# Optimization experiments

Measured on AMD Instinct MI355X. Metric: run time of the kernel, lower is better.

The kernel has to match this reference:

```python
import jax, jax.numpy as jnp
import numpy as np

SCALE = 768.0  # scale = output_features


def setup_inputs() -> dict:
    key = jax.random.key(0)
    k1, k2, k3, k4 = jax.random.split(key, 4)
    B, S, D, F = 8, 2048, 768, 768
    x = jax.random.normal(k1, (B, S, D), dtype=jnp.float32)
    # torch nn.Linear weights: shape (out_features, in_features), y = x @ W.T
    Wq = jax.random.normal(k2, (F, D), dtype=jnp.float32) * (1.0 / np.sqrt(D))
    Wk = jax.random.normal(k3, (F, D), dtype=jnp.float32) * (1.0 / np.sqrt(D))
    Wv = jax.random.normal(k4, (F, D), dtype=jnp.float32) * (1.0 / np.sqrt(D))
    return {"x": x, "Wq": Wq, "Wk": Wk, "Wv": Wv}


def _cdist_l2(q, k):
    # pairwise Euclidean distances, [B, S, S]; matches torch.cdist(q, k, p=2)
    q2 = jnp.sum(q * q, axis=-1)  # [B, S]
    k2 = jnp.sum(k * k, axis=-1)  # [B, S]
    qk = jnp.einsum('bid,bjd->bij', q, k)  # [B, S, S]
    d2 = q2[:, :, None] + k2[:, None, :] - 2.0 * qk
    return jnp.sqrt(jnp.maximum(d2, 0.0))


def reference(x, Wq, Wk, Wv):
    q = jnp.einsum('bsd,fd->bsf', x, Wq)
    k = jnp.einsum('bsd,fd->bsf', x, Wk)
    v = jnp.einsum('bsd,fd->bsf', x, Wv)
    scores = _cdist_l2(q, k) / jnp.sqrt(jnp.asarray(SCALE, dtype=x.dtype))
    attn = jax.nn.softmax(scores, axis=-1)  # NOTE: source softmaxes raw distances (no negation)
    return jnp.einsum('bij,bjf->bif', attn, v)
```

## Files before the change

### kernel.cpp

```cpp
#include <hip/hip_runtime.h>
#include <stdint.h>
#include <math.h>


typedef __attribute__((ext_vector_type(8))) __bf16 bf16x8;
typedef __attribute__((ext_vector_type(4))) float f32x4;

__device__ __forceinline__ unsigned short f2b(float f) {
    unsigned u = __float_as_uint(f);
    unsigned r = 0x7fffu + ((u >> 16) & 1u);
    return (unsigned short)((u + r) >> 16);
}
__device__ __forceinline__ float b2f(unsigned short h) {
    return __uint_as_float(((unsigned)h) << 16);
}

__device__ __forceinline__ void wg_barrier() {
    asm volatile("" ::: "memory");
    __builtin_amdgcn_s_barrier();
    asm volatile("" ::: "memory");
}

__device__ __forceinline__ void glds16(const unsigned short* src, unsigned short* dst) {
    __builtin_amdgcn_global_load_lds(
        (const __attribute__((address_space(1))) unsigned int*)src,
        (__attribute__((address_space(3))) unsigned int*)dst, 16, 0, 0);
}

__device__ __forceinline__ unsigned lds_off(const void* p) {
    return (unsigned)(uintptr_t)(const __attribute__((address_space(3))) char*)p;
}

__global__ __launch_bounds__(256) void castk(const float* __restrict__ src,
                                             unsigned short* __restrict__ dst, int n4) {
    int i = blockIdx.x * 256 + threadIdx.x;
    if (i >= n4) return;
    float4 v = ((const float4*)src)[i];
    ushort4 o;
    o.x = f2b(v.x); o.y = f2b(v.y); o.z = f2b(v.z); o.w = f2b(v.w);
    ((ushort4*)dst)[i] = o;
}

template <int MODE>
__global__ __launch_bounds__(256) void rowreduce(const unsigned short* __restrict__ X,
                                                 int L, int rows, float* __restrict__ out) {
    int w = threadIdx.x >> 6, lane = threadIdx.x & 63;
    int row = blockIdx.x * 4 + w;
    if (row >= rows) return;
    const unsigned short* xr = X + (size_t)row * L;
    float s = 0.f;
    int passes = L >> 8;
    for (int p = 0; p < passes; ++p) {
        ushort4 u = *(const ushort4*)(xr + (p << 8) + lane * 4);
        float a = b2f(u.x), b = b2f(u.y), c = b2f(u.z), d = b2f(u.w);
        s += MODE ? (a * a + b * b + c * c + d * d) : (a + b + c + d);
    }
#pragma unroll
    for (int o = 32; o > 0; o >>= 1) s += __shfl_down(s, o);
    if (lane == 0) out[row] = s;
}

#define MF(A_, B_, C_) (C_) = __builtin_amdgcn_mfma_f32_16x16x32_bf16((A_), (B_), (C_), 0, 0, 0)
#define DSR(dst_, a_, imm_) \
    asm volatile("ds_read_b128 %0, %1 offset:" #imm_ : "=v"(dst_) : "v"(a_))
#define LGKM(n_) asm volatile("s_waitcnt lgkmcnt(" #n_ ")" ::: "memory")
#define VMC6 asm volatile("s_waitcnt vmcnt(6)" ::: "memory")
#define VMC0 asm volatile("s_waitcnt vmcnt(0)" ::: "memory")
#define SB0 __builtin_amdgcn_sched_barrier(0)
#define NOPS ((void)0)

#define CLUSTER(MI0_, NI0_, AARR_, BARR_)                                  \
    _Pragma("unroll") for (int mi_ = 0; mi_ < 4; ++mi_) {                  \
        _Pragma("unroll") for (int ni_ = 0; ni_ < 2; ++ni_) {              \
            MF(AARR_[mi_][0], BARR_[ni_][0], acc[(MI0_) + mi_][(NI0_) + ni_]); \
            MF(AARR_[mi_][1], BARR_[ni_][1], acc[(MI0_) + mi_][(NI0_) + ni_]); \
        }                                                                  \
    }

#define TILE(A0_, A0X_, B0_, B0X_, S1_, S2_, S3_, S4_, VMW_) do {          \
    DSR(aF[0][0], A0_, 0);    DSR(aF[0][1], A0X_, 0);                      \
    DSR(aF[1][0], A0_, 2048); DSR(aF[1][1], A0X_, 2048);                   \
    DSR(aF[2][0], A0_, 4096); DSR(aF[2][1], A0X_, 4096);                   \
    DSR(aF[3][0], A0_, 6144); DSR(aF[3][1], A0X_, 6144);                   \
    DSR(bL[0][0], B0_, 0);    DSR(bL[0][1], B0X_, 0);                      \
    DSR(bL[1][0], B0_, 2048); DSR(bL[1][1], B0X_, 2048);                   \
    S1_;                                                                   \
    LGKM(8);                                                               \
    wg_barrier();                                                          \
    LGKM(0); SB0;                                                          \
    __builtin_amdgcn_s_setprio(1);                                         \
    CLUSTER(0, 0, aF, bL)                                                  \
    SB0; __builtin_amdgcn_s_setprio(0);                                    \
    wg_barrier();                                                          \
    DSR(bH[0][0], B0_, 4096); DSR(bH[0][1], B0X_, 4096);                   \
    DSR(bH[1][0], B0_, 6144); DSR(bH[1][1], B0X_, 6144);                   \
    S2_;                                                                   \
    wg_barrier();                                                          \
    LGKM(0); SB0;                                                          \
    __builtin_amdgcn_s_setprio(1);                                         \
    CLUSTER(0, 2, aF, bH)                                                  \
    SB0; __builtin_amdgcn_s_setprio(0);                                    \
    wg_barrier();                                                          \
    DSR(aH[0][0], A0_, 8192);  DSR(aH[0][1], A0X_, 8192);                  \
    DSR(aH[1][0], A0_, 10240); DSR(aH[1][1], A0X_, 10240);                 \
    DSR(aH[2][0], A0_, 12288); DSR(aH[2][1], A0X_, 12288);                 \
    DSR(aH[3][0], A0_, 14336); DSR(aH[3][1], A0X_, 14336);                 \
    S3_;                                                                   \
    wg_barrier();                                                          \
    LGKM(0); SB0;                                                          \
    __builtin_amdgcn_s_setprio(1);                                         \
    CLUSTER(4, 2, aH, bH)                                                  \
    SB0; __builtin_amdgcn_s_setprio(0);                                    \
    wg_barrier();                                                          \
    S4_;                                                                   \
    VMW_;                                                                  \
    wg_barrier();                                                          \
    SB0;                                                                   \
    __builtin_amdgcn_s_setprio(1);                                         \
    CLUSTER(4, 0, aH, bL)                                                  \
    SB0; __builtin_amdgcn_s_setprio(0);                                    \
    wg_barrier();                                                          \
} while (0)

#define SA_(T_, BUF_, H_) do {                                             \
    const unsigned short* s_ = pA0 + (size_t)((H_) * 64) * lda + (size_t)(T_) * 64; \
    unsigned short* d_ = As + (BUF_) * 16384 + (H_) * 4096 + tid * 8;      \
    glds16(s_, d_);                                                        \
    glds16(s_ + (size_t)128 * lda, d_ + 8192);                             \
} while (0)
#define SBs_(T_, BUF_, H_) do {                                            \
    const unsigned short* s_ = pB0 + (size_t)((H_) * 32) * ldb + (size_t)(T_) * 64; \
    unsigned short* d_ = Bs + (BUF_) * 16384 + (H_) * 2048 + dB0 + tid * 8; \
    glds16(s_, d_);                                                        \
    glds16(s_ + (size_t)128 * ldb, d_ + 8192);                             \
} while (0)

template <int EPI>
__global__ __launch_bounds__(512, 2) void gemm256(
    const unsigned short* __restrict__ A, int lda, long long sA,
    const unsigned short* __restrict__ B, int ldb, long long sB,
    void* __restrict__ Cv, int ldc, long long sC,
    int Kd,
    const float* __restrict__ aux1, int sAux1,
    const float* __restrict__ aux2, int sAux2,
    float invs) {
    __shared__ __attribute__((aligned(128))) unsigned short As[2 * 256 * 64];
    __shared__ __attribute__((aligned(128))) unsigned short Bs[2 * 256 * 64];

    const int z = blockIdx.z;
    const unsigned short* __restrict__ Ab = A + (size_t)z * sA;
    const unsigned short* __restrict__ Bb = B + (size_t)z * sB;
    const int i0 = blockIdx.y * 256;
    const int j0 = blockIdx.x * 256;
    const int tid = threadIdx.x;
    const int w = tid >> 6, lane = tid & 63;
    const int wr = w >> 2, wc = w & 3;
    const int c16 = lane & 15, kq = lane >> 4;

    const int lr0 = tid >> 3;
    const int clog0 = (tid & 7) ^ (lr0 & 7);
    const unsigned short* pA0 = Ab + (size_t)(i0 + lr0) * lda + clog0 * 8;
    const unsigned short* pB0 = Bb + (size_t)(j0 + lr0 + (lr0 & 32)) * ldb + clog0 * 8;
    const int dB0 = (tid & 256) << 3;

    const int swc = (kq ^ (c16 & 7)) << 4;
    const unsigned adrA0 = lds_off(As) + (unsigned)(wr * 128 + c16) * 128 + swc;
    const unsigned adrA0x = adrA0 ^ 64u;
    const unsigned adrA1 = adrA0 + 32768u, adrA1x = adrA0x + 32768u;
    const unsigned adrB0 = lds_off(Bs) + (unsigned)(wc * 64 + c16) * 128 + swc;
    const unsigned adrB0x = adrB0 ^ 64u;
    const unsigned adrB1 = adrB0 + 32768u, adrB1x = adrB0x + 32768u;

    f32x4 acc[8][4];
    const f32x4 zero = {0.f, 0.f, 0.f, 0.f};
#pragma unroll
    for (int i = 0; i < 8; ++i)
#pragma unroll
        for (int j = 0; j < 4; ++j) acc[i][j] = zero;

    bf16x8 aF[4][2], aH[4][2], bL[2][2], bH[2][2];

    const int npairs = Kd >> 7;

    SA_(0, 0, 0); SA_(0, 0, 1); SBs_(0, 0, 0); SBs_(0, 0, 1);
    SA_(1, 1, 0); SBs_(1, 1, 0); SA_(1, 1, 1);
    VMC6;
    wg_barrier();

    for (int u = 0; u < npairs - 1; ++u) {
        const int t0 = 2 * u;
        TILE(adrA0, adrA0x, adrB0, adrB0x,
             SBs_(t0 + 1, 1, 1), SA_(t0 + 2, 0, 0), SBs_(t0 + 2, 0, 0), SA_(t0 + 2, 0, 1),
             VMC6);
        TILE(adrA1, adrA1x, adrB1, adrB1x,
             SBs_(t0 + 2, 0, 1), SA_(t0 + 3, 1, 0), SBs_(t0 + 3, 1, 0), SA_(t0 + 3, 1, 1),
             VMC6);
    }
    {
        const int t0 = 2 * npairs - 2;
        TILE(adrA0, adrA0x, adrB0, adrB0x,
             SBs_(t0 + 1, 1, 1), NOPS, NOPS, NOPS, VMC0);
        TILE(adrA1, adrA1x, adrB1, adrB1x, NOPS, NOPS, NOPS, NOPS, NOPS);
    }

    const int r4 = kq * 4;
    if constexpr (EPI == 0) {
        unsigned short* C = (unsigned short*)Cv + (size_t)z * sC;
#pragma unroll
        for (int mi = 0; mi < 8; ++mi)
#pragma unroll
            for (int ni = 0; ni < 4; ++ni) {
                const int row = i0 + wr * 128 + mi * 16 + r4;
                const int col = j0 + wc * 64 + ni * 16 + c16;
#pragma unroll
                for (int r = 0; r < 4; ++r)
                    C[(size_t)(row + r) * ldc + col] = f2b(acc[mi][ni][r]);
            }
    } else if constexpr (EPI == 1) {
        unsigned short* C = (unsigned short*)Cv + (size_t)z * sC;
        const float* q2b = aux1 + (size_t)z * sAux1;
        const float* k2b = aux2 + (size_t)z * sAux2;
#pragma unroll
        for (int mi = 0; mi < 8; ++mi)
#pragma unroll
            for (int ni = 0; ni < 4; ++ni) {
                const int row = i0 + wr * 128 + mi * 16 + r4;
                const int col = j0 + wc * 64 + ni * 16 + c16;
                const float k2v = k2b[col];
#pragma unroll
                for (int r = 0; r < 4; ++r) {
                    float d2 = q2b[row + r] + k2v - 2.0f * acc[mi][ni][r];
                    float e = __expf(sqrtf(fmaxf(d2, 0.f)) * invs);
                    C[(size_t)(row + r) * ldc + col] = f2b(e);
                }
            }
    } else {
        float* C = (float*)Cv + (size_t)z * sC;
        const float* lb = aux1 + (size_t)z * sAux1;
#pragma unroll
        for (int mi = 0; mi < 8; ++mi)
#pragma unroll
            for (int ni = 0; ni < 4; ++ni) {
                const int row = i0 + wr * 128 + mi * 16 + r4;
                const int col = j0 + wc * 64 + ni * 16 + c16;
#pragma unroll
                for (int r = 0; r < 4; ++r)
                    C[(size_t)(row + r) * ldc + col] = acc[mi][ni][r] / lb[row + r];
            }
    }
}

extern "C" void kernel_launch(void* const* d_in, const int* in_sizes, int n_in,
                              void* d_out, int out_size, void* d_ws, size_t ws_size,
                              hipStream_t stream) {
    const float* x = (const float*)d_in[0];
    const float* Wq = (const float*)d_in[1];
    const float* Wk = (const float*)d_in[2];
    const float* Wv = (const float*)d_in[3];
    const int Bz = 8, S = 2048, D = 768, F = 768;
    const int BS = Bz * S;

    const size_t szX = (size_t)BS * D * 2;
    const size_t szW = (size_t)F * D * 2;
    const size_t szE = (size_t)Bz * S * S * 2;

    char* p = (char*)d_ws;
    unsigned short* xb = (unsigned short*)p;  p += szX;
    unsigned short* Wqb = (unsigned short*)p; p += szW;
    unsigned short* Wkb = (unsigned short*)p; p += szW;
    unsigned short* Wvb = (unsigned short*)p; p += szW;
    unsigned short* Qm = (unsigned short*)p;  p += szX;
    unsigned short* Km = (unsigned short*)p;  p += szX;
    unsigned short* VT = (unsigned short*)p;  p += szX;
    unsigned short* E = (unsigned short*)p;   p += szE;
    float* q2 = (float*)p;   p += (size_t)BS * 4;
    float* k2 = (float*)p;   p += (size_t)BS * 4;
    float* lsum = (float*)p; p += (size_t)BS * 4;
    if ((size_t)(p - (char*)d_ws) > ws_size) return;

    const float invs = 1.0f / sqrtf(768.0f);

    castk<<<(BS * D / 4 + 255) / 256, 256, 0, stream>>>(x, xb, BS * D / 4);
    castk<<<(F * D / 4 + 255) / 256, 256, 0, stream>>>(Wq, Wqb, F * D / 4);
    castk<<<(F * D / 4 + 255) / 256, 256, 0, stream>>>(Wk, Wkb, F * D / 4);
    castk<<<(F * D / 4 + 255) / 256, 256, 0, stream>>>(Wv, Wvb, F * D / 4);

    gemm256<0><<<dim3(F / 256, BS / 256, 2), 512, 0, stream>>>(
        xb, D, 0,
        Wqb, D, (long long)F * D,
        Qm, F, (long long)BS * F,
        D, nullptr, 0, nullptr, 0, 0.f);

    gemm256<0><<<dim3(BS / 256, F / 256, 1), 512, 0, stream>>>(
        Wvb, D, 0,
        xb, D, 0,
        VT, BS, 0,
        D, nullptr, 0, nullptr, 0, 0.f);

    rowreduce<1><<<BS / 4, 256, 0, stream>>>(Qm, F, BS, q2);
    rowreduce<1><<<BS / 4, 256, 0, stream>>>(Km, F, BS, k2);

    gemm256<1><<<dim3(S / 256, S / 256, Bz), 512, 0, stream>>>(
        Qm, F, (long long)S * F,
        Km, F, (long long)S * F,
        E, S, (long long)S * S,
        F, q2, S, k2, S, invs);

    rowreduce<0><<<BS / 4, 256, 0, stream>>>(E, S, BS, lsum);

    gemm256<2><<<dim3(F / 256, S / 256, Bz), 512, 0, stream>>>(
        E, S, (long long)S * S,
        VT, BS, (long long)S,
        d_out, F, (long long)S * F,
        S, lsum, S, nullptr, 0, 0.f);
}
```

Baseline: 262.2 us.

## Shrink GEMM K-tile to 32 with simpler double-buffered pipeline

Replaces the 256x256x64 GEMM main loop, which used a four-phase schedule with staggered half-tile prefetches and partial vmcnt waits, with a 256x256x32 tile. Each step prefetches the whole next tile and waits on vmcnt(0) at the end of the step. LDS use per block is halved, which may allow more blocks per CU, and the control flow is simpler. In exchange the number of barriers per unit of K doubles and the prefetch depth is shallower, which can expose global load latency.

Measured after the change: 280.4 us. 1.07x slower.

```diff
diff --git a/kernel.cpp b/kernel.cpp
--- a/kernel.cpp
+++ b/kernel.cpp
@@ -63,76 +63,49 @@
 #define MF(A_, B_, C_) (C_) = __builtin_amdgcn_mfma_f32_16x16x32_bf16((A_), (B_), (C_), 0, 0, 0)
 #define DSR(dst_, a_, imm_) \
     asm volatile("ds_read_b128 %0, %1 offset:" #imm_ : "=v"(dst_) : "v"(a_))
-#define LGKM(n_) asm volatile("s_waitcnt lgkmcnt(" #n_ ")" ::: "memory")
-#define VMC6 asm volatile("s_waitcnt vmcnt(6)" ::: "memory")
+#define LGKM0 asm volatile("s_waitcnt lgkmcnt(0)" ::: "memory")
 #define VMC0 asm volatile("s_waitcnt vmcnt(0)" ::: "memory")
 #define SB0 __builtin_amdgcn_sched_barrier(0)
-#define NOPS ((void)0)
-
-#define CLUSTER(MI0_, NI0_, AARR_, BARR_)                                  \
-    _Pragma("unroll") for (int mi_ = 0; mi_ < 4; ++mi_) {                  \
-        _Pragma("unroll") for (int ni_ = 0; ni_ < 2; ++ni_) {              \
-            MF(AARR_[mi_][0], BARR_[ni_][0], acc[(MI0_) + mi_][(NI0_) + ni_]); \
-            MF(AARR_[mi_][1], BARR_[ni_][1], acc[(MI0_) + mi_][(NI0_) + ni_]); \
-        }                                                                  \
-    }
-
-#define TILE(A0_, A0X_, B0_, B0X_, S1_, S2_, S3_, S4_, VMW_) do {          \
-    DSR(aF[0][0], A0_, 0);    DSR(aF[0][1], A0X_, 0);                      \
-    DSR(aF[1][0], A0_, 2048); DSR(aF[1][1], A0X_, 2048);                   \
-    DSR(aF[2][0], A0_, 4096); DSR(aF[2][1], A0X_, 4096);                   \
-    DSR(aF[3][0], A0_, 6144); DSR(aF[3][1], A0X_, 6144);                   \
-    DSR(bL[0][0], B0_, 0);    DSR(bL[0][1], B0X_, 0);                      \
-    DSR(bL[1][0], B0_, 2048); DSR(bL[1][1], B0X_, 2048);                   \
-    S1_;                                                                   \
-    LGKM(8);                                                               \
-    wg_barrier();                                                          \
-    LGKM(0); SB0;                                                          \
+
+#define SA_(T_, BUFW_) do {                                                \
+    const unsigned short* s_ = pA0 + (size_t)(T_) * 32;                    \
+    unsigned short* d_ = As + (BUFW_) * 8192 + tid * 8;                    \
+    glds16(s_, d_);                                                        \
+    glds16(s_ + (size_t)128 * lda, d_ + 4096);                             \
+} while (0)
+#define SB_(T_, BUFW_) do {                                                \
+    const unsigned short* s_ = pB0 + (size_t)(T_) * 32;                    \
+    unsigned short* d_ = Bs + (BUFW_) * 8192 + tid * 8;                    \
+    glds16(s_, d_);                                                        \
+    glds16(s_ + (size_t)128 * ldb, d_ + 4096);                             \
+} while (0)
+
+#define TILE(AD_, BD_, T_, BUFW_) do {                                     \
+    bf16x8 af[4], ah[4], bv[4];                                            \
+    DSR(af[0], AD_, 0);    DSR(af[1], AD_, 1024);                          \
+    DSR(af[2], AD_, 2048); DSR(af[3], AD_, 3072);                          \
+    DSR(bv[0], BD_, 0);    DSR(bv[1], BD_, 1024);                          \
+    DSR(bv[2], BD_, 2048); DSR(bv[3], BD_, 3072);                          \
+    if ((T_) + 1 < nt) { SA_((T_) + 1, BUFW_); SB_((T_) + 1, BUFW_); }     \
+    wg_barrier();                                                          \
+    LGKM0; SB0;                                                            \
     __builtin_amdgcn_s_setprio(1);                                         \
-    CLUSTER(0, 0, aF, bL)                                                  \
+    _Pragma("unroll") for (int mi_ = 0; mi_ < 4; ++mi_)                    \
+        _Pragma("unroll") for (int ni_ = 0; ni_ < 4; ++ni_)                \
+            MF(af[mi_], bv[ni_], acc[mi_][ni_]);                           \
     SB0; __builtin_amdgcn_s_setprio(0);                                    \
     wg_barrier();                                                          \
-    DSR(bH[0][0], B0_, 4096); DSR(bH[0][1], B0X_, 4096);                   \
-    DSR(bH[1][0], B0_, 6144); DSR(bH[1][1], B0X_, 6144);                   \
-    S2_;                                                                   \
-    wg_barrier();                                                          \
-    LGKM(0); SB0;                                                          \
+    DSR(ah[0], AD_, 4096); DSR(ah[1], AD_, 5120);                          \
+    DSR(ah[2], AD_, 6144); DSR(ah[3], AD_, 7168);                          \
+    wg_barrier();                                                          \
+    LGKM0; SB0;                                                            \
     __builtin_amdgcn_s_setprio(1);                                         \
-    CLUSTER(0, 2, aF, bH)                                                  \
+    _Pragma("unroll") for (int mi_ = 0; mi_ < 4; ++mi_)                    \
+        _Pragma("unroll") for (int ni_ = 0; ni_ < 4; ++ni_)                \
+            MF(ah[mi_], bv[ni_], acc[4 + mi_][ni_]);                       \
     SB0; __builtin_amdgcn_s_setprio(0);                                    \
-    wg_barrier();                                                          \
-    DSR(aH[0][0], A0_, 8192);  DSR(aH[0][1], A0X_, 8192);                  \
-    DSR(aH[1][0], A0_, 10240); DSR(aH[1][1], A0X_, 10240);                 \
-    DSR(aH[2][0], A0_, 12288); DSR(aH[2][1], A0X_, 12288);                 \
-    DSR(aH[3][0], A0_, 14336); DSR(aH[3][1], A0X_, 14336);                 \
-    S3_;                                                                   \
-    wg_barrier();                                                          \
-    LGKM(0); SB0;                                                          \
-    __builtin_amdgcn_s_setprio(1);                                         \
-    CLUSTER(4, 2, aH, bH)                                                  \
-    SB0; __builtin_amdgcn_s_setprio(0);                                    \
-    wg_barrier();                                                          \
-    S4_;                                                                   \
-    VMW_;                                                                  \
-    wg_barrier();                                                          \
-    SB0;                                                                   \
-    __builtin_amdgcn_s_setprio(1);                                         \
-    CLUSTER(4, 0, aH, bL)                                                  \
-    SB0; __builtin_amdgcn_s_setprio(0);                                    \
-    wg_barrier();                                                          \
-} while (0)
-
-#define SA_(T_, BUF_, H_) do {                                             \
-    const unsigned short* s_ = pA0 + (size_t)((H_) * 64) * lda + (size_t)(T_) * 64; \
-    unsigned short* d_ = As + (BUF_) * 16384 + (H_) * 4096 + tid * 8;      \
-    glds16(s_, d_);                                                        \
-    glds16(s_ + (size_t)128 * lda, d_ + 8192);                             \
-} while (0)
-#define SBs_(T_, BUF_, H_) do {                                            \
-    const unsigned short* s_ = pB0 + (size_t)((H_) * 32) * ldb + (size_t)(T_) * 64; \
-    unsigned short* d_ = Bs + (BUF_) * 16384 + (H_) * 2048 + dB0 + tid * 8; \
-    glds16(s_, d_);                                                        \
-    glds16(s_ + (size_t)128 * ldb, d_ + 8192);                             \
+    VMC0;                                                                  \
+    wg_barrier();                                                          \
 } while (0)
 
 template <int EPI>
@@ -144,8 +117,8 @@
     const float* __restrict__ aux1, int sAux1,
     const float* __restrict__ aux2, int sAux2,
     float invs) {
-    __shared__ __attribute__((aligned(128))) unsigned short As[2 * 256 * 64];
-    __shared__ __attribute__((aligned(128))) unsigned short Bs[2 * 256 * 64];
+    __shared__ __attribute__((aligned(128))) unsigned short As[2 * 256 * 32];
+    __shared__ __attribute__((aligned(128))) unsigned short Bs[2 * 256 * 32];
 
     const int z = blockIdx.z;
     const unsigned short* __restrict__ Ab = A + (size_t)z * sA;
@@ -157,19 +130,16 @@
     const int wr = w >> 2, wc = w & 3;
     const int c16 = lane & 15, kq = lane >> 4;
 
-    const int lr0 = tid >> 3;
-    const int clog0 = (tid & 7) ^ (lr0 & 7);
-    const unsigned short* pA0 = Ab + (size_t)(i0 + lr0) * lda + clog0 * 8;
-    const unsigned short* pB0 = Bb + (size_t)(j0 + lr0 + (lr0 & 32)) * ldb + clog0 * 8;
-    const int dB0 = (tid & 256) << 3;
-
-    const int swc = (kq ^ (c16 & 7)) << 4;
-    const unsigned adrA0 = lds_off(As) + (unsigned)(wr * 128 + c16) * 128 + swc;
-    const unsigned adrA0x = adrA0 ^ 64u;
-    const unsigned adrA1 = adrA0 + 32768u, adrA1x = adrA0x + 32768u;
-    const unsigned adrB0 = lds_off(Bs) + (unsigned)(wc * 64 + c16) * 128 + swc;
-    const unsigned adrB0x = adrB0 ^ 64u;
-    const unsigned adrB1 = adrB0 + 32768u, adrB1x = adrB0x + 32768u;
+    const int srow = tid >> 2;
+    const int clog = (tid & 3) ^ ((tid >> 3) & 3);
+    const unsigned short* pA0 = Ab + (size_t)(i0 + srow) * lda + clog * 8;
+    const unsigned short* pB0 = Bb + (size_t)(j0 + srow) * ldb + clog * 8;
+
+    const int swc = (kq ^ ((c16 >> 1) & 3)) << 4;
+    const unsigned adrA0 = lds_off(As) + (unsigned)(wr * 128 + c16) * 64 + swc;
+    const unsigned adrA1 = adrA0 + 16384u;
+    const unsigned adrB0 = lds_off(Bs) + (unsigned)(wc * 64 + c16) * 64 + swc;
+    const unsigned adrB1 = adrB0 + 16384u;
 
     f32x4 acc[8][4];
     const f32x4 zero = {0.f, 0.f, 0.f, 0.f};
@@ -178,29 +148,15 @@
 #pragma unroll
         for (int j = 0; j < 4; ++j) acc[i][j] = zero;
 
-    bf16x8 aF[4][2], aH[4][2], bL[2][2], bH[2][2];
-
-    const int npairs = Kd >> 7;
-
-    SA_(0, 0, 0); SA_(0, 0, 1); SBs_(0, 0, 0); SBs_(0, 0, 1);
-    SA_(1, 1, 0); SBs_(1, 1, 0); SA_(1, 1, 1);
-    VMC6;
+    const int nt = Kd >> 5;
+
+    SA_(0, 0); SB_(0, 0);
+    VMC0;
     wg_barrier();
 
-    for (int u = 0; u < npairs - 1; ++u) {
-        const int t0 = 2 * u;
-        TILE(adrA0, adrA0x, adrB0, adrB0x,
-             SBs_(t0 + 1, 1, 1), SA_(t0 + 2, 0, 0), SBs_(t0 + 2, 0, 0), SA_(t0 + 2, 0, 1),
-             VMC6);
-        TILE(adrA1, adrA1x, adrB1, adrB1x,
-             SBs_(t0 + 2, 0, 1), SA_(t0 + 3, 1, 0), SBs_(t0 + 3, 1, 0), SA_(t0 + 3, 1, 1),
-             VMC6);
-    }
-    {
-        const int t0 = 2 * npairs - 2;
-        TILE(adrA0, adrA0x, adrB0, adrB0x,
-             SBs_(t0 + 1, 1, 1), NOPS, NOPS, NOPS, VMC0);
-        TILE(adrA1, adrA1x, adrB1, adrB1x, NOPS, NOPS, NOPS, NOPS, NOPS);
+    for (int t = 0; t < nt; t += 2) {
+        TILE(adrA0, adrB0, t, 1);
+        TILE(adrA1, adrB1, t + 1, 0);
     }
 
     const int r4 = kq * 4;
```
